# Kernel optimization log

Hardware: AMD Instinct MI355X
Metric: run time of the kernel (lower is better)

The kernel has to match this reference:

```python
import jax, jax.numpy as jnp
import numpy as np

F = 256  # filters
FQ = F // 8  # query/key channels


def setup_inputs() -> dict:
    key = jax.random.key(0)
    ks = jax.random.split(key, 9)
    B, H, W = 4, 64, 64
    s_in = 1.0 / np.sqrt(F)
    inp = {
        "inputs": jax.random.normal(ks[0], (B, H, W, F), jnp.float32),
        "Wq": jax.random.normal(ks[1], (F, FQ), jnp.float32) * s_in,
        "bq": jnp.zeros((FQ,), jnp.float32),
        "Wk": jax.random.normal(ks[2], (F, FQ), jnp.float32) * s_in,
        "bk": jnp.zeros((FQ,), jnp.float32),
        "Wv": jax.random.normal(ks[3], (F, F), jnp.float32) * s_in,
        "bv": jnp.zeros((F,), jnp.float32),
        "Wo": jax.random.normal(ks[4], (F, F), jnp.float32) * s_in,
        "bo": jnp.zeros((F,), jnp.float32),
    }
    return inp


def reference(inputs, Wq, bq, Wk, bk, Wv, bv, Wo, bo):
    B, H, W, C = inputs.shape
    N = H * W
    x = inputs.reshape(B, N, C)  # 1x1 conv == per-token linear
    q = jax.nn.relu(jnp.einsum('bnc,cd->bnd', x, Wq) + bq)  # [B,N,FQ]
    k = jax.nn.relu(jnp.einsum('bnc,cd->bnd', x, Wk) + bk)  # [B,N,FQ]
    v = jax.nn.relu(jnp.einsum('bnc,cd->bnd', x, Wv) + bv)  # [B,N,C]
    # unscaled full attention (as in the original module)
    attn = jax.nn.softmax(jnp.einsum('bnd,bmd->bnm', q, k), axis=-1)  # [B,N,N]
    attended = jnp.einsum('bnm,bmc->bnc', attn, v)  # [B,N,C]
    out = jax.nn.relu(jnp.einsum('bnc,cd->bnd', attended, Wo) + bo)
    return inputs + out.reshape(B, H, W, C)
```

## Files before the change

### kernel.cpp

```cpp
#include <hip/hip_runtime.h>

typedef __attribute__((ext_vector_type(8))) short short8;
typedef __attribute__((ext_vector_type(4))) float floatx4;
typedef __attribute__((ext_vector_type(2))) unsigned int uintx2;
typedef __attribute__((ext_vector_type(4))) unsigned int uintx4;

#define MFMA16(a, b, c) __builtin_amdgcn_mfma_f32_16x16x32_bf16((a), (b), (c), 0, 0, 0)

#define LDP 80
#define LDO 264
#define LOG2E 1.4426950408889634f
#define PSHIFT 23.083120654223414f

__device__ __forceinline__ float bf2f(unsigned short u) {
  return __uint_as_float(((unsigned int)u) << 16);
}
__device__ __forceinline__ unsigned short f2bf(float f) {
  unsigned int x = __float_as_uint(f);
  x += 0x7FFFu + ((x >> 16) & 1u);
  return (unsigned short)(x >> 16);
}
__device__ __forceinline__ unsigned int cvt_pk_bf16(float lo, float hi) {
  unsigned int r;
  asm("v_cvt_pk_bf16_f32 %0, %1, %2" : "=v"(r) : "v"(lo), "v"(hi));
  return r;
}
__device__ __forceinline__ float ld_in(const void* p, long i, int isf32) {
  if (isf32) return ((const float*)p)[i];
  return bf2f(((const unsigned short*)p)[i]);
}
__device__ __forceinline__ short8 ld16(const unsigned short* p) {
  return *(const short8*)__builtin_assume_aligned(p, 16);
}
__device__ __forceinline__ void st16(unsigned short* p, short8 v) {
  *(short8*)__builtin_assume_aligned(p, 16) = v;
}
__device__ __forceinline__ int detect_bad(const unsigned short* x, int idx) {
  const short8 v = ld16(x + (long)idx * 8);
  int bad = 0;
#pragma unroll
  for (int j = 0; j < 8; j++) {
    const unsigned int e = (((unsigned short)v[j]) >> 7) & 0xFFu;
    if (e >= 141u) bad = 1;
  }
  return bad;
}


__global__ __launch_bounds__(256)
void prep_kernel(const void* __restrict__ x,
                 const void* __restrict__ Wq, const void* __restrict__ Wk,
                 const void* __restrict__ Wv, const void* __restrict__ Wo,
                 unsigned short* __restrict__ Wf_qk,
                 unsigned short* __restrict__ Wf_v,
                 unsigned short* __restrict__ Wf_o,
                 int* __restrict__ flagout) {
  __shared__ unsigned short Vl[64][LDP];
  __shared__ int flagl[4];
  const int t = (int)threadIdx.x;
  const int wave = t >> 6, lane = t & 63;
  {
    const int bad = detect_bad((const unsigned short*)x, t) |
                    detect_bad((const unsigned short*)x, 256 + t);
    if (lane == 0) flagl[wave] = (__ballot(bad) != 0ull) ? 1 : 0;
  }
  __syncthreads();
  const int isf32 = flagl[0] | flagl[1] | flagl[2] | flagl[3];
  if (t == 0) flagout[0] = isf32;

  const int blk = (int)blockIdx.x;
  const int j = t & 63, r4 = t >> 6;

  if (blk < 32) {
    const void* W = (blk < 16) ? Wo : Wv;
    unsigned short* dst = (blk < 16) ? Wf_o : Wf_v;
    const int b2 = blk & 15;
    const int g0 = (b2 >> 2) * 64, c0 = (b2 & 3) * 64;
#pragma unroll
    for (int k2 = 0; k2 < 16; k2++) {
      const int rr = r4 * 16 + k2;
      Vl[j][rr] = f2bf(ld_in(W, (long)(c0 + rr) * 256 + g0 + j, isf32));
    }
    __syncthreads();
#pragma unroll
    for (int cc = 0; cc < 2; cc++) {
      const int c = t + cc * 256;
      const int f_l = c >> 6, lane_c = c & 63;
      const int og = f_l >> 1, kse = f_l & 1;
      const int out_l = lane_c & 15, q = lane_c >> 4;
      const short8 v = ld16(&Vl[og * 16 + out_l][kse * 32 + q * 8]);
      st16(dst + (long)(((g0 >> 4) + og) * 8 + (c0 >> 5) + kse) * 512 + lane_c * 8, v);
    }
  } else {
    const int c0 = (blk - 32) * 64;
#pragma unroll
    for (int k2 = 0; k2 < 16; k2++) {
      const int cl = r4 * 16 + k2;
      const float v = (j < 32) ? ld_in(Wq, (long)(c0 + cl) * 32 + j, isf32) * LOG2E
                               : ld_in(Wk, (long)(c0 + cl) * 32 + (j - 32), isf32);
      Vl[j][cl] = f2bf(v);
    }
    __syncthreads();
#pragma unroll
    for (int cc = 0; cc < 2; cc++) {
      const int c = t + cc * 256;
      const int f_l = c >> 6, lane_c = c & 63;
      const int og = f_l >> 1, kse = f_l & 1;
      const int out_l = lane_c & 15, q = lane_c >> 4;
      const short8 v = ld16(&Vl[og * 16 + out_l][kse * 32 + q * 8]);
      st16(Wf_qk + (long)(og * 8 + (c0 >> 5) + kse) * 512 + lane_c * 8, v);
    }
  }
}

__global__ __launch_bounds__(256)
void proj_kernel(const void* __restrict__ x,
                 const void* __restrict__ bq, const void* __restrict__ bk,
                 const void* __restrict__ bv,
                 const unsigned short* __restrict__ Wf_qk,
                 const unsigned short* __restrict__ Wf_v,
                 const int* __restrict__ flag,
                 unsigned short* __restrict__ Qf, unsigned short* __restrict__ Kf,
                 unsigned short* __restrict__ Vf) {
  __shared__ unsigned short Vl[64][LDP];
  const int t = (int)threadIdx.x;
  const int wave = t >> 6, lane = t & 63, quad = lane >> 4, l15 = lane & 15;

  const int isf32 = flag[0];

  const int blk = (int)blockIdx.x;
  const int ct = blk >> 8;
  const long row_base = (long)(blk & 255) * 64;
  const long arow = row_base + wave * 16 + l15;

  const unsigned short* wb = (ct == 0) ? Wf_qk
                                       : (Wf_v + (long)(ct - 1) * 4 * 8 * 512);

  floatx4 acc[4];
  acc[0] = acc[1] = acc[2] = acc[3] = (floatx4)0.0f;

#pragma unroll
  for (int ks = 0; ks < 8; ks++) {
    short8 a;
    if (isf32) {
      const float* xf = (const float*)x + arow * 256 + ks * 32 + quad * 8;
      const floatx4 f0 = *(const floatx4*)xf;
      const floatx4 f1 = *(const floatx4*)(xf + 4);
      uintx4 u;
      u[0] = cvt_pk_bf16(f0[0], f0[1]); u[1] = cvt_pk_bf16(f0[2], f0[3]);
      u[2] = cvt_pk_bf16(f1[0], f1[1]); u[3] = cvt_pk_bf16(f1[2], f1[3]);
      a = *(short8*)&u;
    } else {
      a = ld16((const unsigned short*)x + arow * 256 + ks * 32 + quad * 8);
    }
#pragma unroll
    for (int tn = 0; tn < 4; tn++) {
      const short8 bfr = ld16(wb + (long)(tn * 8 + ks) * 512 + lane * 8);
      acc[tn] = MFMA16(a, bfr, acc[tn]);
    }
  }

  if (ct == 0) {
#pragma unroll
    for (int tn = 0; tn < 4; tn++) {
      const int g = tn * 16 + l15;
      const float bias = (g < 32) ? ld_in(bq, g, isf32) * LOG2E
                                  : ld_in(bk, g - 32, isf32);
#pragma unroll
      for (int r = 0; r < 4; r++)
        Vl[wave * 16 + quad * 4 + r][g] = f2bf(fmaxf(acc[tn][r] + bias, 0.0f));
    }
    __syncthreads();
    const long f0 = row_base >> 4;
#pragma unroll
    for (int cc = 0; cc < 2; cc++) {
      const int c = t + cc * 256;
      const int isK = c >> 8;
      const int c2 = c & 255;
      const int f_l = c2 >> 6, lane_c = c2 & 63;
      const int row_l = lane_c & 15, q = lane_c >> 4;
      const short8 v = ld16(&Vl[f_l * 16 + row_l][isK * 32 + q * 8]);
      unsigned short* dst = isK ? Kf : Qf;
      st16(dst + (f0 + f_l) * 512 + lane_c * 8, v);
    }
  } else {
#pragma unroll
    for (int tn = 0; tn < 4; tn++) {
      const float bias = ld_in(bv, (long)(ct - 1) * 64 + tn * 16 + l15, isf32);
#pragma unroll
      for (int r = 0; r < 4; r++)
        Vl[tn * 16 + l15][wave * 16 + quad * 4 + r] =
            f2bf(fmaxf(acc[tn][r] + bias, 0.0f));
    }
    __syncthreads();
    const long bb = row_base >> 12;
    const int kt = (int)((row_base & 4095) >> 6);
    const long fbase = (bb * 64 + kt) * 32 + (long)(ct - 1) * 8;
#pragma unroll
    for (int cc = 0; cc < 2; cc++) {
      const int c = t * 2 + cc;
      const int f_l = c >> 6, lane_c = c & 63;
      const int cg = f_l >> 1, kh = f_l & 1;
      const int ch_l = lane_c & 15, q = lane_c >> 4;
      const short8 v = ld16(&Vl[cg * 16 + ch_l][kh * 32 + q * 8]);
      st16(Vf + (fbase + f_l) * 512 + lane_c * 8, v);
    }
  }
}

__global__ __launch_bounds__(512, 2)
void flash_kernel(const unsigned short* __restrict__ Qf,
                  const unsigned short* __restrict__ Kf,
                  const unsigned short* __restrict__ Vf,
                  const unsigned short* __restrict__ Wf_o,
                  const void* __restrict__ bo,
                  const void* __restrict__ xin, void* __restrict__ out) {
  __shared__ unsigned short Pl[2][64 * LDP];
  __shared__ unsigned short Ol[64 * LDO];
  __shared__ float Lp[2][64];
  __shared__ float Ll[64];
  __shared__ int flagl[8];

  const int t = (int)threadIdx.x;
  const int wave = t >> 6, lane = t & 63, quad = lane >> 4, l15 = lane & 15;

  {
    const int bad = detect_bad((const unsigned short*)xin, t);
    if (lane == 0) flagl[wave] = (__ballot(bad) != 0ull) ? 1 : 0;
  }

  const int raw = (int)blockIdx.x;
  const int b = raw & 3;
  const int mt = raw >> 2;
  const long qrow0 = (long)b * 4096 + (long)mt * 64;
  const int m = wave & 3, h = wave >> 2;

  const long kfrag0 = (long)b * 256;
  const long vfrag0 = (long)b * 64 * 32;

  const short8 qf = ld16(Qf + ((qrow0 >> 4) + m) * 512 + lane * 8);

  floatx4 oacc[4][2];
#pragma unroll
  for (int i = 0; i < 4; i++) { oacc[i][0] = (floatx4)0.0f; oacc[i][1] = (floatx4)0.0f; }
  float lpart = 0.0f;

  short8 kb[2];
#pragma unroll
  for (int i = 0; i < 2; i++)
    kb[i] = ld16(Kf + (kfrag0 + h * 2 + i) * 512 + lane * 8);
  {
    floatx4 s[2];
#pragma unroll
    for (int i = 0; i < 2; i++) { s[i] = (floatx4)0.0f; s[i] = MFMA16(kb[i], qf, s[i]); }
    unsigned short* pl = Pl[0];
#pragma unroll
    for (int i = 0; i < 2; i++) {
      const float p0 = exp2f(s[i][0] - PSHIFT);
      const float p1 = exp2f(s[i][1] - PSHIFT);
      const float p2 = exp2f(s[i][2] - PSHIFT);
      const float p3 = exp2f(s[i][3] - PSHIFT);
      lpart += (p0 + p1) + (p2 + p3);
      uintx2 w;
      w[0] = cvt_pk_bf16(p0, p1);
      w[1] = cvt_pk_bf16(p2, p3);
      *(uintx2*)__builtin_assume_aligned(
          &pl[(m * 16 + l15) * LDP + h * 32 + i * 16 + quad * 4], 8) = w;
    }
  }
#pragma unroll
  for (int i = 0; i < 2; i++)
    kb[i] = ld16(Kf + (kfrag0 + 4 + h * 2 + i) * 512 + lane * 8);
  __syncthreads();

  for (int kt = 0; kt < 64; kt++) {
    short8 vb[2][2];
#pragma unroll
    for (int tv = 0; tv < 2; tv++)
#pragma unroll
      for (int kh = 0; kh < 2; kh++)
        vb[tv][kh] = ld16(Vf + (vfrag0 + (long)kt * 32 + (wave * 2 + tv) * 2 + kh) * 512 + lane * 8);

    const unsigned short* plr = Pl[kt & 1];
    short8 pa[4][2];
#pragma unroll
    for (int rm = 0; rm < 4; rm++)
#pragma unroll
      for (int kh = 0; kh < 2; kh++)
        pa[rm][kh] = ld16(&plr[(rm * 16 + l15) * LDP + kh * 32 + quad * 8]);

    short8 kbn[2];
    const int kt2 = (kt + 2) & 63;
#pragma unroll
    for (int i = 0; i < 2; i++)
      kbn[i] = ld16(Kf + (kfrag0 + kt2 * 4 + h * 2 + i) * 512 + lane * 8);

    if (kt < 63) {
      floatx4 s[2];
#pragma unroll
      for (int i = 0; i < 2; i++) { s[i] = (floatx4)0.0f; s[i] = MFMA16(kb[i], qf, s[i]); }
      unsigned short* pl = Pl[(kt + 1) & 1];
#pragma unroll
      for (int i = 0; i < 2; i++) {
        const float p0 = exp2f(s[i][0] - PSHIFT);
        const float p1 = exp2f(s[i][1] - PSHIFT);
        const float p2 = exp2f(s[i][2] - PSHIFT);
        const float p3 = exp2f(s[i][3] - PSHIFT);
        lpart += (p0 + p1) + (p2 + p3);
        uintx2 w;
        w[0] = cvt_pk_bf16(p0, p1);
        w[1] = cvt_pk_bf16(p2, p3);
        *(uintx2*)__builtin_assume_aligned(
            &pl[(m * 16 + l15) * LDP + h * 32 + i * 16 + quad * 4], 8) = w;
      }
    }
    kb[0] = kbn[0]; kb[1] = kbn[1];

    __builtin_amdgcn_s_setprio(1);
#pragma unroll
    for (int kh = 0; kh < 2; kh++)
#pragma unroll
      for (int tv = 0; tv < 2; tv++)
#pragma unroll
        for (int rm = 0; rm < 4; rm++)
          oacc[rm][tv] = MFMA16(pa[rm][kh], vb[tv][kh], oacc[rm][tv]);
    __builtin_amdgcn_s_setprio(0);
    __syncthreads();
  }

  lpart += __shfl_xor(lpart, 16);
  lpart += __shfl_xor(lpart, 32);
  if (lane < 16) Lp[h][m * 16 + lane] = lpart;
  __syncthreads();
  if (t < 64) Ll[t] = 1.0f / (Lp[0][t] + Lp[1][t]);
  __syncthreads();

#pragma unroll
  for (int rm = 0; rm < 4; rm++) {
    const floatx4 ll = *(const floatx4*)&Ll[rm * 16 + quad * 4];
#pragma unroll
    for (int tv = 0; tv < 2; tv++)
#pragma unroll
      for (int r = 0; r < 4; r++)
        Ol[(rm * 16 + quad * 4 + r) * LDO + wave * 32 + tv * 16 + l15] =
            f2bf(oacc[rm][tv][r] * ll[r]);
  }
  __syncthreads();

  const int isf32 = flagl[0] | flagl[1] | flagl[2] | flagl[3] |
                    flagl[4] | flagl[5] | flagl[6] | flagl[7];
  const int m2 = wave & 3, gh = wave >> 2;
  floatx4 acc2[8];
#pragma unroll
  for (int i = 0; i < 8; i++) acc2[i] = (floatx4)0.0f;
#pragma unroll
  for (int ks = 0; ks < 8; ks++) {
    const short8 a = ld16(&Ol[(m2 * 16 + l15) * LDO + ks * 32 + quad * 8]);
#pragma unroll
    for (int tn = 0; tn < 8; tn++) {
      const short8 bfr = ld16(Wf_o + (long)((gh * 8 + tn) * 8 + ks) * 512 + lane * 8);
      acc2[tn] = MFMA16(a, bfr, acc2[tn]);
    }
  }
  __syncthreads();
#pragma unroll
  for (int tn = 0; tn < 8; tn++) {
    const int g = gh * 128 + tn * 16 + l15;
    const float bias = ld_in(bo, g, isf32);
#pragma unroll
    for (int r = 0; r < 4; r++)
      Ol[(m2 * 16 + quad * 4 + r) * LDO + g] = f2bf(fmaxf(acc2[tn][r] + bias, 0.0f));
  }
  __syncthreads();

  if (isf32) {
    const float* xf = (const float*)xin + qrow0 * 256;
    float* of = (float*)out + qrow0 * 256;
#pragma unroll
    for (int p = 0; p < 8; p++) {
      const int idx = p * 2048 + t * 4;
      const int row = idx >> 8, ch = idx & 255;
      floatx4 xv = *(const floatx4*)(xf + idx);
      floatx4 ov;
#pragma unroll
      for (int j = 0; j < 4; j++) ov[j] = bf2f(Ol[row * LDO + ch + j]) + xv[j];
      *(floatx4*)(of + idx) = ov;
    }
  } else {
    const unsigned short* xh = (const unsigned short*)xin + qrow0 * 256;
    unsigned short* oh = (unsigned short*)out + qrow0 * 256;
#pragma unroll
    for (int p = 0; p < 4; p++) {
      const int idx = p * 4096 + t * 8;
      const int row = idx >> 8, ch = idx & 255;
      const short8 xv = ld16(xh + idx);
      short8 ov;
#pragma unroll
      for (int j = 0; j < 8; j++)
        ov[j] = (short)f2bf(bf2f(Ol[row * LDO + ch + j]) + bf2f((unsigned short)xv[j]));
      st16(oh + idx, ov);
    }
  }
}

extern "C" void kernel_launch(void* const* d_in, const int* in_sizes, int n_in,
                              void* d_out, int out_size, void* d_ws, size_t ws_size,
                              hipStream_t stream) {
  const void* x  = d_in[0];
  const void* Wq = d_in[1]; const void* bq = d_in[2];
  const void* Wk = d_in[3]; const void* bk = d_in[4];
  const void* Wv = d_in[5]; const void* bv = d_in[6];
  const void* Wo = d_in[7]; const void* bo = d_in[8];

  char* ws = (char*)d_ws;
  unsigned short* Qf    = (unsigned short*)ws;
  unsigned short* Kf    = Qf + (long)4 * 4096 * 32;
  unsigned short* Vf    = Kf + (long)4 * 4096 * 32;
  unsigned short* Wf_o  = Vf + (long)4 * 256 * 4096;
  unsigned short* Wf_v  = Wf_o + (long)128 * 512;
  unsigned short* Wf_qk = Wf_v + (long)128 * 512;
  int* flag             = (int*)(Wf_qk + (long)32 * 512);

  prep_kernel<<<36, 256, 0, stream>>>(x, Wq, Wk, Wv, Wo, Wf_qk, Wf_v, Wf_o, flag);
  proj_kernel<<<1280, 256, 0, stream>>>(x, bq, bk, bv, Wf_qk, Wf_v, flag, Qf, Kf, Vf);
  flash_kernel<<<256, 512, 0, stream>>>(Qf, Kf, Vf, Wf_o, bo, x, d_out);
}
```

Baseline: 166.5 us.

## Split flash loop into producer waves for softmax and consumer waves for PV MFMA

Restructures the attention loop into warp specialization: waves 0-3 compute QK^T scores, exp and P tiles for a full 64-key block each, while waves 4-7 only load V and run the P·V MFMAs over 64 output channels each. Previously every wave did both halves of the work. The aim is to overlap transcendental/VALU work with matrix work across waves. In exchange, consumer waves hold twice as many accumulators (16 floatx4), which raises register pressure, and the per-iteration barrier still couples the two groups, so any imbalance between them becomes idle time.

Measured after the change: 172.8 us. +3.8%, slower.

```diff
diff --git a/kernel.cpp b/kernel.cpp
--- a/kernel.cpp
+++ b/kernel.cpp
@@ -217,7 +217,7 @@
                   const void* __restrict__ xin, void* __restrict__ out) {
   __shared__ unsigned short Pl[2][64 * LDP];
   __shared__ unsigned short Ol[64 * LDO];
-  __shared__ float Lp[2][64];
+  __shared__ float Lpr[64];
   __shared__ float Ll[64];
   __shared__ int flagl[8];
 
@@ -233,117 +233,128 @@
   const int b = raw & 3;
   const int mt = raw >> 2;
   const long qrow0 = (long)b * 4096 + (long)mt * 64;
-  const int m = wave & 3, h = wave >> 2;
+  const int isProd = (wave < 4);
+  const int p = wave & 3;
 
   const long kfrag0 = (long)b * 256;
   const long vfrag0 = (long)b * 64 * 32;
 
-  const short8 qf = ld16(Qf + ((qrow0 >> 4) + m) * 512 + lane * 8);
-
-  floatx4 oacc[4][2];
-#pragma unroll
-  for (int i = 0; i < 4; i++) { oacc[i][0] = (floatx4)0.0f; oacc[i][1] = (floatx4)0.0f; }
   float lpart = 0.0f;
-
-  short8 kb[2];
-#pragma unroll
-  for (int i = 0; i < 2; i++)
-    kb[i] = ld16(Kf + (kfrag0 + h * 2 + i) * 512 + lane * 8);
-  {
-    floatx4 s[2];
-#pragma unroll
-    for (int i = 0; i < 2; i++) { s[i] = (floatx4)0.0f; s[i] = MFMA16(kb[i], qf, s[i]); }
-    unsigned short* pl = Pl[0];
-#pragma unroll
-    for (int i = 0; i < 2; i++) {
-      const float p0 = exp2f(s[i][0] - PSHIFT);
-      const float p1 = exp2f(s[i][1] - PSHIFT);
-      const float p2 = exp2f(s[i][2] - PSHIFT);
-      const float p3 = exp2f(s[i][3] - PSHIFT);
-      lpart += (p0 + p1) + (p2 + p3);
-      uintx2 w;
-      w[0] = cvt_pk_bf16(p0, p1);
-      w[1] = cvt_pk_bf16(p2, p3);
-      *(uintx2*)__builtin_assume_aligned(
-          &pl[(m * 16 + l15) * LDP + h * 32 + i * 16 + quad * 4], 8) = w;
-    }
-  }
-#pragma unroll
-  for (int i = 0; i < 2; i++)
-    kb[i] = ld16(Kf + (kfrag0 + 4 + h * 2 + i) * 512 + lane * 8);
-  __syncthreads();
-
-  for (int kt = 0; kt < 64; kt++) {
-    short8 vb[2][2];
-#pragma unroll
-    for (int tv = 0; tv < 2; tv++)
-#pragma unroll
-      for (int kh = 0; kh < 2; kh++)
-        vb[tv][kh] = ld16(Vf + (vfrag0 + (long)kt * 32 + (wave * 2 + tv) * 2 + kh) * 512 + lane * 8);
-
-    const unsigned short* plr = Pl[kt & 1];
-    short8 pa[4][2];
-#pragma unroll
-    for (int rm = 0; rm < 4; rm++)
-#pragma unroll
-      for (int kh = 0; kh < 2; kh++)
-        pa[rm][kh] = ld16(&plr[(rm * 16 + l15) * LDP + kh * 32 + quad * 8]);
-
-    short8 kbn[2];
-    const int kt2 = (kt + 2) & 63;
-#pragma unroll
-    for (int i = 0; i < 2; i++)
-      kbn[i] = ld16(Kf + (kfrag0 + kt2 * 4 + h * 2 + i) * 512 + lane * 8);
-
-    if (kt < 63) {
-      floatx4 s[2];
-#pragma unroll
-      for (int i = 0; i < 2; i++) { s[i] = (floatx4)0.0f; s[i] = MFMA16(kb[i], qf, s[i]); }
-      unsigned short* pl = Pl[(kt + 1) & 1];
-#pragma unroll
-      for (int i = 0; i < 2; i++) {
-        const float p0 = exp2f(s[i][0] - PSHIFT);
-        const float p1 = exp2f(s[i][1] - PSHIFT);
-        const float p2 = exp2f(s[i][2] - PSHIFT);
-        const float p3 = exp2f(s[i][3] - PSHIFT);
+  floatx4 oacc[4][4];
+#pragma unroll
+  for (int i = 0; i < 4; i++)
+#pragma unroll
+    for (int j = 0; j < 4; j++) oacc[i][j] = (floatx4)0.0f;
+
+  short8 qf, kb[4];
+  if (isProd) {
+    qf = ld16(Qf + ((qrow0 >> 4) + p) * 512 + lane * 8);
+#pragma unroll
+    for (int j = 0; j < 4; j++)
+      kb[j] = ld16(Kf + (kfrag0 + j) * 512 + lane * 8);
+    {
+      floatx4 s[4];
+#pragma unroll
+      for (int j = 0; j < 4; j++) { s[j] = (floatx4)0.0f; s[j] = MFMA16(kb[j], qf, s[j]); }
+      unsigned short* pl = Pl[0];
+#pragma unroll
+      for (int j = 0; j < 4; j++) {
+        const float p0 = exp2f(s[j][0] - PSHIFT);
+        const float p1 = exp2f(s[j][1] - PSHIFT);
+        const float p2 = exp2f(s[j][2] - PSHIFT);
+        const float p3 = exp2f(s[j][3] - PSHIFT);
         lpart += (p0 + p1) + (p2 + p3);
         uintx2 w;
         w[0] = cvt_pk_bf16(p0, p1);
         w[1] = cvt_pk_bf16(p2, p3);
         *(uintx2*)__builtin_assume_aligned(
-            &pl[(m * 16 + l15) * LDP + h * 32 + i * 16 + quad * 4], 8) = w;
+            &pl[(p * 16 + l15) * LDP + j * 16 + quad * 4], 8) = w;
       }
     }
-    kb[0] = kbn[0]; kb[1] = kbn[1];
-
-    __builtin_amdgcn_s_setprio(1);
-#pragma unroll
-    for (int kh = 0; kh < 2; kh++)
-#pragma unroll
-      for (int tv = 0; tv < 2; tv++)
-#pragma unroll
-        for (int rm = 0; rm < 4; rm++)
-          oacc[rm][tv] = MFMA16(pa[rm][kh], vb[tv][kh], oacc[rm][tv]);
-    __builtin_amdgcn_s_setprio(0);
+#pragma unroll
+    for (int j = 0; j < 4; j++)
+      kb[j] = ld16(Kf + (kfrag0 + 4 + j) * 512 + lane * 8);
+  }
+  __syncthreads();
+
+  for (int kt = 0; kt < 64; kt++) {
+    if (!isProd) {
+      short8 vb[4][2];
+#pragma unroll
+      for (int tn = 0; tn < 4; tn++)
+#pragma unroll
+        for (int kh = 0; kh < 2; kh++)
+          vb[tn][kh] = ld16(Vf + (vfrag0 + (long)kt * 32 + (p * 4 + tn) * 2 + kh) * 512 + lane * 8);
+
+      const unsigned short* plr = Pl[kt & 1];
+      short8 pa[4][2];
+#pragma unroll
+      for (int rm = 0; rm < 4; rm++)
+#pragma unroll
+        for (int kh = 0; kh < 2; kh++)
+          pa[rm][kh] = ld16(&plr[(rm * 16 + l15) * LDP + kh * 32 + quad * 8]);
+
+      __builtin_amdgcn_s_setprio(1);
+#pragma unroll
+      for (int kh = 0; kh < 2; kh++)
+#pragma unroll
+        for (int tn = 0; tn < 4; tn++)
+#pragma unroll
+          for (int rm = 0; rm < 4; rm++)
+            oacc[rm][tn] = MFMA16(pa[rm][kh], vb[tn][kh], oacc[rm][tn]);
+      __builtin_amdgcn_s_setprio(0);
+    } else {
+      short8 kbn[4];
+      const int kt2 = (kt + 2) & 63;
+#pragma unroll
+      for (int j = 0; j < 4; j++)
+        kbn[j] = ld16(Kf + (kfrag0 + kt2 * 4 + j) * 512 + lane * 8);
+
+      if (kt < 63) {
+        floatx4 s[4];
+#pragma unroll
+        for (int j = 0; j < 4; j++) { s[j] = (floatx4)0.0f; s[j] = MFMA16(kb[j], qf, s[j]); }
+        unsigned short* pl = Pl[(kt + 1) & 1];
+#pragma unroll
+        for (int j = 0; j < 4; j++) {
+          const float p0 = exp2f(s[j][0] - PSHIFT);
+          const float p1 = exp2f(s[j][1] - PSHIFT);
+          const float p2 = exp2f(s[j][2] - PSHIFT);
+          const float p3 = exp2f(s[j][3] - PSHIFT);
+          lpart += (p0 + p1) + (p2 + p3);
+          uintx2 w;
+          w[0] = cvt_pk_bf16(p0, p1);
+          w[1] = cvt_pk_bf16(p2, p3);
+          *(uintx2*)__builtin_assume_aligned(
+              &pl[(p * 16 + l15) * LDP + j * 16 + quad * 4], 8) = w;
+        }
+      }
+#pragma unroll
+      for (int j = 0; j < 4; j++) kb[j] = kbn[j];
+    }
     __syncthreads();
   }
 
-  lpart += __shfl_xor(lpart, 16);
-  lpart += __shfl_xor(lpart, 32);
-  if (lane < 16) Lp[h][m * 16 + lane] = lpart;
-  __syncthreads();
-  if (t < 64) Ll[t] = 1.0f / (Lp[0][t] + Lp[1][t]);
-  __syncthreads();
-
-#pragma unroll
-  for (int rm = 0; rm < 4; rm++) {
-    const floatx4 ll = *(const floatx4*)&Ll[rm * 16 + quad * 4];
-#pragma unroll
-    for (int tv = 0; tv < 2; tv++)
-#pragma unroll
-      for (int r = 0; r < 4; r++)
-        Ol[(rm * 16 + quad * 4 + r) * LDO + wave * 32 + tv * 16 + l15] =
-            f2bf(oacc[rm][tv][r] * ll[r]);
+  if (isProd) {
+    lpart += __shfl_xor(lpart, 16);
+    lpart += __shfl_xor(lpart, 32);
+    if (lane < 16) Lpr[p * 16 + lane] = lpart;
+  }
+  __syncthreads();
+  if (t < 64) Ll[t] = 1.0f / Lpr[t];
+  __syncthreads();
+
+  if (!isProd) {
+#pragma unroll
+    for (int rm = 0; rm < 4; rm++) {
+      const floatx4 ll = *(const floatx4*)&Ll[rm * 16 + quad * 4];
+#pragma unroll
+      for (int tn = 0; tn < 4; tn++)
+#pragma unroll
+        for (int r = 0; r < 4; r++)
+          Ol[(rm * 16 + quad * 4 + r) * LDO + p * 64 + tn * 16 + l15] =
+              f2bf(oacc[rm][tn][r] * ll[r]);
+    }
   }
   __syncthreads();
 
@@ -377,8 +388,8 @@
     const float* xf = (const float*)xin + qrow0 * 256;
     float* of = (float*)out + qrow0 * 256;
 #pragma unroll
-    for (int p = 0; p < 8; p++) {
-      const int idx = p * 2048 + t * 4;
+    for (int pp = 0; pp < 8; pp++) {
+      const int idx = pp * 2048 + t * 4;
       const int row = idx >> 8, ch = idx & 255;
       floatx4 xv = *(const floatx4*)(xf + idx);
       floatx4 ov;
@@ -390,8 +401,8 @@
     const unsigned short* xh = (const unsigned short*)xin + qrow0 * 256;
     unsigned short* oh = (unsigned short*)out + qrow0 * 256;
 #pragma unroll
-    for (int p = 0; p < 4; p++) {
-      const int idx = p * 4096 + t * 8;
+    for (int pp = 0; pp < 4; pp++) {
+      const int idx = pp * 4096 + t * 8;
       const int row = idx >> 8, ch = idx & 255;
       const short8 xv = ld16(xh + idx);
       short8 ov;
```
